# Optimization experiments

Measured on AMD Instinct MI355X. Metric: run time of the kernel, lower is better.

Reference implementation:

```python
import jax, jax.numpy as jnp
import numpy as np

NEG_BIG = -9e15


def setup_inputs() -> dict:
    key = jax.random.key(0)
    k1, k2, k3, k4 = jax.random.split(key, 4)
    B, N, F_in, F_out = 8, 2048, 512, 256
    x = jax.random.normal(k1, (B, N, F_in), dtype=jnp.float32)
    adj = jax.random.randint(k2, (B, N, N), 0, 2, dtype=jnp.int32)
    W = jax.random.normal(k3, (F_in, F_out), dtype=jnp.float32) * (1.414 / np.sqrt(F_in))
    a = jax.random.normal(k4, (2 * F_out, 1), dtype=jnp.float32) * 0.1
    return {"x": x, "adj": adj, "W": W, "a": a}


def reference(x, adj, W, a):
    # x: [B,N,Fin], adj: [B,N,N] int mask, W: [Fin,Fout], a: [2*Fout,1]
    alpha = 0.2  # LeakyReLU negative slope
    F_out = W.shape[1]
    h = jnp.einsum('bnf,fo->bno', x, W)              # [B,N,Fout]
    a1 = a[:F_out, 0]                                # [Fout]
    a2 = a[F_out:, 0]                                # [Fout]
    # e_ij = LeakyReLU([h_i || h_j] . a) = LeakyReLU(h_i.a1 + h_j.a2)
    f = h @ a1                                       # [B,N]
    g = h @ a2                                       # [B,N]
    e = jax.nn.leaky_relu(f[:, :, None] + g[:, None, :], negative_slope=alpha)  # [B,N,N]
    e = jnp.where(adj > 0, e, NEG_BIG)
    attention = jax.nn.softmax(e, axis=2)            # row-wise over neighbors j
    h_prime = jnp.einsum('bij,bjo->bio', attention, h)  # [B,N,Fout]
    return jax.nn.elu(h_prime)                       # concat=True path
```

## Files before the change

### kernel.cpp

```cpp
#include <hip/hip_runtime.h>
#include <math.h>

#define BATCH 8
#define NN    2048
#define FIN   512
#define FOUT  256
#define NEG_BIG -9000000000000000.0f

typedef __attribute__((ext_vector_type(8))) short bf16x8;
typedef __attribute__((ext_vector_type(4))) float f32x4;

__device__ __forceinline__ unsigned short f2bf(float x) {
    unsigned u = __float_as_uint(x);
    u = (u + 0x7FFF + ((u >> 16) & 1)) >> 16;
    return (unsigned short)u;
}
__device__ __forceinline__ float bf2f(unsigned short h) {
    return __uint_as_float(((unsigned)h) << 16);
}

__global__ __launch_bounds__(256) void wt_prep(const float* __restrict__ W,
                                               unsigned short* __restrict__ Wt_hi,
                                               unsigned short* __restrict__ Wt_lo) {
    const int tg = blockIdx.x * 256 + threadIdx.x;
    const int n  = tg >> 7;
    const int k4 = (tg & 127) * 4;
    unsigned short h[4], lo[4];
    #pragma unroll
    for (int i = 0; i < 4; i++) {
        const float v = W[(size_t)(k4 + i) * FOUT + n];
        h[i]  = f2bf(v);
        lo[i] = f2bf(v - bf2f(h[i]));
    }
    uint2 ph, pl;
    ph.x = h[0]  | ((unsigned)h[1]  << 16); ph.y = h[2]  | ((unsigned)h[3]  << 16);
    pl.x = lo[0] | ((unsigned)lo[1] << 16); pl.y = lo[2] | ((unsigned)lo[3] << 16);
    *(uint2*)(Wt_hi + (size_t)n * FIN + k4) = ph;
    *(uint2*)(Wt_lo + (size_t)n * FIN + k4) = pl;
}

__global__ __launch_bounds__(256, 2) void gemm_xw(const float* __restrict__ x,
        const unsigned short* __restrict__ Wt_hi,
        const unsigned short* __restrict__ Wt_lo,
        unsigned short* __restrict__ ht_hi,
        unsigned short* __restrict__ ht_lo) {
    __shared__ unsigned short As_hi[128][40];
    __shared__ unsigned short As_lo[128][40];
    const int t  = threadIdx.x;
    const int m0 = (blockIdx.x >> 2) * 128;
    const int n0 = (blockIdx.x & 3) * 64;
    const int l  = t & 63, w = t >> 6;
    const int wr = w >> 1, wc = w & 1;
    const int lr = l & 15, lk = l >> 4;

    f32x4 acc[4][2];
    #pragma unroll
    for (int mt = 0; mt < 4; mt++)
        #pragma unroll
        for (int nt = 0; nt < 2; nt++) acc[mt][nt] = (f32x4){0.f,0.f,0.f,0.f};

    for (int k0 = 0; k0 < FIN; k0 += 32) {
        float4 xv[4];
        #pragma unroll
        for (int r = 0; r < 4; r++) {
            const int fidx = t + 256*r, m = fidx >> 3, kq = fidx & 7;
            xv[r] = *(const float4*)(x + (size_t)(m0 + m) * FIN + k0 + kq*4);
        }
        bf16x8 bh[2], bl[2];
        #pragma unroll
        for (int nt = 0; nt < 2; nt++) {
            const size_t off = (size_t)(n0 + wc*32 + nt*16 + lr) * FIN + k0 + lk*8;
            bh[nt] = *(const bf16x8*)(Wt_hi + off);
            bl[nt] = *(const bf16x8*)(Wt_lo + off);
        }
        __syncthreads();
        #pragma unroll
        for (int r = 0; r < 4; r++) {
            const int fidx = t + 256*r, m = fidx >> 3, kq = fidx & 7;
            const float vv[4] = {xv[r].x, xv[r].y, xv[r].z, xv[r].w};
            unsigned short h[4], lo[4];
            #pragma unroll
            for (int i = 0; i < 4; i++) { h[i] = f2bf(vv[i]); lo[i] = f2bf(vv[i] - bf2f(h[i])); }
            uint2 ph, pl;
            ph.x = h[0]  | ((unsigned)h[1]  << 16); ph.y = h[2]  | ((unsigned)h[3]  << 16);
            pl.x = lo[0] | ((unsigned)lo[1] << 16); pl.y = lo[2] | ((unsigned)lo[3] << 16);
            *(uint2*)&As_hi[m][kq*4] = ph;
            *(uint2*)&As_lo[m][kq*4] = pl;
        }
        __syncthreads();
        bf16x8 ah[4], al[4];
        #pragma unroll
        for (int mt = 0; mt < 4; mt++) {
            const int row = wr*64 + mt*16 + lr;
            ah[mt] = *(const bf16x8*)&As_hi[row][lk*8];
            al[mt] = *(const bf16x8*)&As_lo[row][lk*8];
        }
        #pragma unroll
        for (int nt = 0; nt < 2; nt++)
            #pragma unroll
            for (int mt = 0; mt < 4; mt++)
                acc[mt][nt] = __builtin_amdgcn_mfma_f32_16x16x32_bf16(ah[mt], bh[nt], acc[mt][nt], 0, 0, 0);
        #pragma unroll
        for (int nt = 0; nt < 2; nt++)
            #pragma unroll
            for (int mt = 0; mt < 4; mt++)
                acc[mt][nt] = __builtin_amdgcn_mfma_f32_16x16x32_bf16(ah[mt], bl[nt], acc[mt][nt], 0, 0, 0);
        #pragma unroll
        for (int nt = 0; nt < 2; nt++)
            #pragma unroll
            for (int mt = 0; mt < 4; mt++)
                acc[mt][nt] = __builtin_amdgcn_mfma_f32_16x16x32_bf16(al[mt], bh[nt], acc[mt][nt], 0, 0, 0);
    }

    #pragma unroll
    for (int mt = 0; mt < 4; mt++)
        #pragma unroll
        for (int nt = 0; nt < 2; nt++) {
            const int n  = n0 + wc*32 + nt*16 + lr;
            const int mb = m0 + wr*64 + mt*16 + lk*4;
            const int bb = mb >> 11, jj = mb & 2047;
            const float av[4] = {acc[mt][nt].x, acc[mt][nt].y, acc[mt][nt].z, acc[mt][nt].w};
            unsigned short h[4], lo[4];
            #pragma unroll
            for (int r = 0; r < 4; r++) { h[r] = f2bf(av[r]); lo[r] = f2bf(av[r] - bf2f(h[r])); }
            uint2 ph, pl;
            ph.x = h[0]  | ((unsigned)h[1]  << 16); ph.y = h[2]  | ((unsigned)h[3]  << 16);
            pl.x = lo[0] | ((unsigned)lo[1] << 16); pl.y = lo[2] | ((unsigned)lo[3] << 16);
            const size_t base = ((size_t)bb * FOUT + n) * NN + jj;
            *(uint2*)(ht_hi + base) = ph;
            *(uint2*)(ht_lo + base) = pl;
        }
}

__global__ __launch_bounds__(256) void fg2(const unsigned short* __restrict__ ht_hi,
                                           const unsigned short* __restrict__ ht_lo,
                                           const float* __restrict__ a,
                                           float* __restrict__ f, float* __restrict__ g) {
    const int lane  = threadIdx.x & 63;
    const int chunk = blockIdx.x * 4 + (threadIdx.x >> 6);
    const int b  = chunk >> 5;
    const int jw = (chunk & 31) * 64 + lane;
    const size_t base = (size_t)b * FOUT * NN + jw;
    float fs = 0.f, gs = 0.f;
    #pragma unroll 4
    for (int n = 0; n < FOUT; n++) {
        const float hv = bf2f(ht_hi[base + (size_t)n * NN]) + bf2f(ht_lo[base + (size_t)n * NN]);
        fs = fmaf(hv, a[n], fs);
        gs = fmaf(hv, a[FOUT + n], gs);
    }
    f[b * NN + jw] = fs;
    g[b * NN + jw] = gs;
}

__global__ __launch_bounds__(256, 1) void gat_attn(
        const unsigned short* __restrict__ ht_hi,
        const unsigned short* __restrict__ ht_lo,
        const int* __restrict__ adj,
        const float* __restrict__ f, const float* __restrict__ g,
        float* __restrict__ out) {
    __shared__ unsigned short Hs_hi[256][72];
    __shared__ unsigned short Hs_lo[256][72];
    __shared__ unsigned short Ps_hi[64][72];
    __shared__ unsigned short Ps_lo[64][72];
    __shared__ __attribute__((aligned(16))) float m_s[64];
    __shared__ __attribute__((aligned(16))) float l_s[64];
    __shared__ __attribute__((aligned(16))) float fac_s[64];

    const int b  = blockIdx.x & 7;
    const int i0 = (blockIdx.x >> 3) * 64;
    const int t  = threadIdx.x;
    const int w  = t >> 6, l = t & 63;
    const int lr = l & 15, lk = l >> 4;
    const int ar = t >> 2, jg = t & 3;
    const float fi = f[b * NN + i0 + ar];

    if (t < 64) { m_s[t] = -INFINITY; l_s[t] = 0.f; }

    f32x4 acc[4][4];
    #pragma unroll
    for (int mt = 0; mt < 4; mt++)
        #pragma unroll
        for (int nt = 0; nt < 4; nt++) acc[mt][nt] = (f32x4){0.f,0.f,0.f,0.f};

    const unsigned short* hb_hi = ht_hi + (size_t)b * FOUT * NN;
    const unsigned short* hb_lo = ht_lo + (size_t)b * FOUT * NN;

    for (int jt = 0; jt < 32; jt++) {
        const int j0 = jt * 64;
        __syncthreads();

        {
            const int sn = t >> 3, sp = t & 7;
            #pragma unroll
            for (int p8 = 0; p8 < 8; p8++) {
                const int n = sn + p8 * 32;
                const size_t goff = (size_t)n * NN + j0 + sp * 8;
                const uint4 vh = *(const uint4*)(hb_hi + goff);
                const uint4 vl = *(const uint4*)(hb_lo + goff);
                *(uint4*)&Hs_hi[n][sp * 8] = vh;
                *(uint4*)&Hs_lo[n][sp * 8] = vl;
            }
        }

        {
            float s[16];
            float mloc = -INFINITY;
            const size_t arow = ((size_t)b * NN + i0 + ar) * NN + j0 + jg * 16;
            #pragma unroll
            for (int c = 0; c < 4; c++) {
                const int4   av = *(const int4*)(adj + arow + c * 4);
                const float4 gv = *(const float4*)(g + b * NN + j0 + jg * 16 + c * 4);
                const float v0 = fi + gv.x, v1 = fi + gv.y, v2 = fi + gv.z, v3 = fi + gv.w;
                s[c*4+0] = av.x > 0 ? (v0 > 0.f ? v0 : 0.2f * v0) : NEG_BIG;
                s[c*4+1] = av.y > 0 ? (v1 > 0.f ? v1 : 0.2f * v1) : NEG_BIG;
                s[c*4+2] = av.z > 0 ? (v2 > 0.f ? v2 : 0.2f * v2) : NEG_BIG;
                s[c*4+3] = av.w > 0 ? (v3 > 0.f ? v3 : 0.2f * v3) : NEG_BIG;
            }
            #pragma unroll
            for (int e = 0; e < 16; e++) mloc = fmaxf(mloc, s[e]);
            mloc = fmaxf(mloc, __shfl_xor(mloc, 1));
            mloc = fmaxf(mloc, __shfl_xor(mloc, 2));
            const float m_old = m_s[ar];
            const float m_new = fmaxf(m_old, mloc);
            float p[16], rs = 0.f;
            #pragma unroll
            for (int e = 0; e < 16; e++) { p[e] = __expf(s[e] - m_new); rs += p[e]; }
            rs += __shfl_xor(rs, 1);
            rs += __shfl_xor(rs, 2);
            if (jg == 0) {
                const float fac = __expf(m_old - m_new);
                fac_s[ar] = fac;
                l_s[ar]   = l_s[ar] * fac + rs;
                m_s[ar]   = m_new;
            }
            unsigned ph[8], pl[8];
            #pragma unroll
            for (int e = 0; e < 16; e += 2) {
                const unsigned short h0 = f2bf(p[e]),   h1 = f2bf(p[e+1]);
                const unsigned short q0 = f2bf(p[e] - bf2f(h0));
                const unsigned short q1 = f2bf(p[e+1] - bf2f(h1));
                ph[e >> 1] = h0 | ((unsigned)h1 << 16);
                pl[e >> 1] = q0 | ((unsigned)q1 << 16);
            }
            *(uint4*)&Ps_hi[ar][jg*16]     = make_uint4(ph[0], ph[1], ph[2], ph[3]);
            *(uint4*)&Ps_hi[ar][jg*16 + 8] = make_uint4(ph[4], ph[5], ph[6], ph[7]);
            *(uint4*)&Ps_lo[ar][jg*16]     = make_uint4(pl[0], pl[1], pl[2], pl[3]);
            *(uint4*)&Ps_lo[ar][jg*16 + 8] = make_uint4(pl[4], pl[5], pl[6], pl[7]);
        }
        __syncthreads();

        #pragma unroll
        for (int mt = 0; mt < 4; mt++) {
            const f32x4 fac4 = *(const f32x4*)&fac_s[mt*16 + lk*4];
            #pragma unroll
            for (int nt = 0; nt < 4; nt++) acc[mt][nt] *= fac4;
        }
        #pragma unroll
        for (int kt = 0; kt < 2; kt++) {
            bf16x8 ah[4], al[4], bh[4], bl[4];
            #pragma unroll
            for (int mt = 0; mt < 4; mt++) {
                ah[mt] = *(const bf16x8*)&Ps_hi[mt*16 + lr][kt*32 + lk*8];
                al[mt] = *(const bf16x8*)&Ps_lo[mt*16 + lr][kt*32 + lk*8];
            }
            #pragma unroll
            for (int nt = 0; nt < 4; nt++) {
                const int n = w*64 + nt*16 + lr;
                bh[nt] = *(const bf16x8*)&Hs_hi[n][kt*32 + lk*8];
                bl[nt] = *(const bf16x8*)&Hs_lo[n][kt*32 + lk*8];
            }
            #pragma unroll
            for (int nt = 0; nt < 4; nt++)
                #pragma unroll
                for (int mt = 0; mt < 4; mt++)
                    acc[mt][nt] = __builtin_amdgcn_mfma_f32_16x16x32_bf16(ah[mt], bh[nt], acc[mt][nt], 0, 0, 0);
            #pragma unroll
            for (int nt = 0; nt < 4; nt++)
                #pragma unroll
                for (int mt = 0; mt < 4; mt++)
                    acc[mt][nt] = __builtin_amdgcn_mfma_f32_16x16x32_bf16(ah[mt], bl[nt], acc[mt][nt], 0, 0, 0);
            #pragma unroll
            for (int nt = 0; nt < 4; nt++)
                #pragma unroll
                for (int mt = 0; mt < 4; mt++)
                    acc[mt][nt] = __builtin_amdgcn_mfma_f32_16x16x32_bf16(al[mt], bh[nt], acc[mt][nt], 0, 0, 0);
        }
    }

    __syncthreads();
    #pragma unroll
    for (int mt = 0; mt < 4; mt++) {
        const f32x4 lv = *(const f32x4*)&l_s[mt*16 + lk*4];
        const float linv[4] = {1.f/lv.x, 1.f/lv.y, 1.f/lv.z, 1.f/lv.w};
        const float av0[4][4] = {
            {acc[mt][0].x, acc[mt][0].y, acc[mt][0].z, acc[mt][0].w},
            {acc[mt][1].x, acc[mt][1].y, acc[mt][1].z, acc[mt][1].w},
            {acc[mt][2].x, acc[mt][2].y, acc[mt][2].z, acc[mt][2].w},
            {acc[mt][3].x, acc[mt][3].y, acc[mt][3].z, acc[mt][3].w}};
        #pragma unroll
        for (int nt = 0; nt < 4; nt++) {
            const int n = w*64 + nt*16 + lr;
            #pragma unroll
            for (int r = 0; r < 4; r++) {
                float v = av0[nt][r] * linv[r];
                v = v > 0.f ? v : (__expf(v) - 1.f);
                out[((size_t)(b * NN + i0 + mt*16 + lk*4 + r)) * FOUT + n] = v;
            }
        }
    }
}

extern "C" void kernel_launch(void* const* d_in, const int* in_sizes, int n_in,
                              void* d_out, int out_size, void* d_ws, size_t ws_size,
                              hipStream_t stream) {
    const float* x   = (const float*)d_in[0];
    const int*   adj = (const int*)  d_in[1];
    const float* W   = (const float*)d_in[2];
    const float* a   = (const float*)d_in[3];
    float* outp = (float*)d_out;

    char* ws = (char*)d_ws;
    unsigned short* ht_hi = (unsigned short*)ws;                       ws += (size_t)BATCH*FOUT*NN*2;
    unsigned short* ht_lo = (unsigned short*)ws;                       ws += (size_t)BATCH*FOUT*NN*2;
    unsigned short* Wt_hi = (unsigned short*)ws;                       ws += (size_t)FOUT*FIN*2;
    unsigned short* Wt_lo = (unsigned short*)ws;                       ws += (size_t)FOUT*FIN*2;
    float* f = (float*)ws;                                             ws += (size_t)BATCH*NN*4;
    float* g = (float*)ws;

    wt_prep <<<128, 256, 0, stream>>>(W, Wt_hi, Wt_lo);
    gemm_xw <<<512, 256, 0, stream>>>(x, Wt_hi, Wt_lo, ht_hi, ht_lo);
    fg2     <<<64,  256, 0, stream>>>(ht_hi, ht_lo, a, f, g);
    gat_attn<<<256, 256, 0, stream>>>(ht_hi, ht_lo, adj, f, g, outp);
}
```

Measured before the change: 354.5 us.

## Use 512-thread attention blocks with direct-to-LDS loads, swizzled LDS and prefetched adjacency

The attention kernel now runs 8 waves per block in a 2x4 wave grid. It stages the H tile with global_load_lds straight into XOR-swizzled unpadded LDS, and register-prefetches the next adjacency and g tile while the MFMAs run. The GEMM epilogue now transposes through LDS so the ht stores are 16-byte coalesced rows instead of scattered 8-byte writes. The aim is higher occupancy, fewer bank conflicts and overlap of the adjacency stream with compute, at the cost of more registers and extra barriers.

New measurement: 320.5 us. -9.6%, faster.

```diff
diff --git a/kernel.cpp b/kernel.cpp
--- a/kernel.cpp
+++ b/kernel.cpp
@@ -17,6 +17,11 @@
 }
 __device__ __forceinline__ float bf2f(unsigned short h) {
     return __uint_as_float(((unsigned)h) << 16);
+}
+__device__ __forceinline__ void gload_lds16(const void* g, void* l) {
+    __builtin_amdgcn_global_load_lds((const __attribute__((address_space(1))) void*)g,
+                                     (__attribute__((address_space(3))) void*)l,
+                                     16, 0, 0);
 }
 
 __global__ __launch_bounds__(256) void wt_prep(const float* __restrict__ W,
@@ -46,6 +51,7 @@
         unsigned short* __restrict__ ht_lo) {
     __shared__ unsigned short As_hi[128][40];
     __shared__ unsigned short As_lo[128][40];
+    __shared__ __attribute__((aligned(16))) unsigned short Tr[64][136];
     const int t  = threadIdx.x;
     const int m0 = (blockIdx.x >> 2) * 128;
     const int n0 = (blockIdx.x & 3) * 64;
@@ -112,24 +118,35 @@
                 acc[mt][nt] = __builtin_amdgcn_mfma_f32_16x16x32_bf16(al[mt], bh[nt], acc[mt][nt], 0, 0, 0);
     }
 
-    #pragma unroll
-    for (int mt = 0; mt < 4; mt++)
-        #pragma unroll
-        for (int nt = 0; nt < 2; nt++) {
-            const int n  = n0 + wc*32 + nt*16 + lr;
-            const int mb = m0 + wr*64 + mt*16 + lk*4;
-            const int bb = mb >> 11, jj = mb & 2047;
-            const float av[4] = {acc[mt][nt].x, acc[mt][nt].y, acc[mt][nt].z, acc[mt][nt].w};
-            unsigned short h[4], lo[4];
-            #pragma unroll
-            for (int r = 0; r < 4; r++) { h[r] = f2bf(av[r]); lo[r] = f2bf(av[r] - bf2f(h[r])); }
-            uint2 ph, pl;
-            ph.x = h[0]  | ((unsigned)h[1]  << 16); ph.y = h[2]  | ((unsigned)h[3]  << 16);
-            pl.x = lo[0] | ((unsigned)lo[1] << 16); pl.y = lo[2] | ((unsigned)lo[3] << 16);
-            const size_t base = ((size_t)bb * FOUT + n) * NN + jj;
-            *(uint2*)(ht_hi + base) = ph;
-            *(uint2*)(ht_lo + base) = pl;
-        }
+    const int bb  = m0 >> 11;
+    const int jj0 = m0 & 2047;
+    for (int pass = 0; pass < 2; pass++) {
+        #pragma unroll
+        for (int mt = 0; mt < 4; mt++)
+            #pragma unroll
+            for (int nt = 0; nt < 2; nt++) {
+                const int nl = wc*32 + nt*16 + lr;
+                const int ml = wr*64 + mt*16 + lk*4;
+                const float vv[4] = {acc[mt][nt].x, acc[mt][nt].y, acc[mt][nt].z, acc[mt][nt].w};
+                unsigned short s[4];
+                #pragma unroll
+                for (int r = 0; r < 4; r++) {
+                    const unsigned short hh = f2bf(vv[r]);
+                    s[r] = pass ? f2bf(vv[r] - bf2f(hh)) : hh;
+                }
+                *(unsigned*)&Tr[nl][ml]     = s[0] | ((unsigned)s[1] << 16);
+                *(unsigned*)&Tr[nl][ml + 2] = s[2] | ((unsigned)s[3] << 16);
+            }
+        __syncthreads();
+        unsigned short* dst = pass ? ht_lo : ht_hi;
+        #pragma unroll
+        for (int q = 0; q < 4; q++) {
+            const int idx = t + 256*q, row = idx >> 4, c = idx & 15;
+            *(uint4*)(dst + ((size_t)(bb * FOUT + n0 + row)) * NN + jj0 + c*8) =
+                *(const uint4*)&Tr[row][c*8];
+        }
+        __syncthreads();
+    }
 }
 
 __global__ __launch_bounds__(256) void fg2(const unsigned short* __restrict__ ht_hi,
@@ -152,16 +169,16 @@
     g[b * NN + jw] = gs;
 }
 
-__global__ __launch_bounds__(256, 1) void gat_attn(
+__global__ __launch_bounds__(512, 1) void gat_attn(
         const unsigned short* __restrict__ ht_hi,
         const unsigned short* __restrict__ ht_lo,
         const int* __restrict__ adj,
         const float* __restrict__ f, const float* __restrict__ g,
         float* __restrict__ out) {
-    __shared__ unsigned short Hs_hi[256][72];
-    __shared__ unsigned short Hs_lo[256][72];
-    __shared__ unsigned short Ps_hi[64][72];
-    __shared__ unsigned short Ps_lo[64][72];
+    __shared__ __attribute__((aligned(16))) unsigned short Hs_hi[256*64];
+    __shared__ __attribute__((aligned(16))) unsigned short Hs_lo[256*64];
+    __shared__ __attribute__((aligned(16))) unsigned short Ps_hi[64*64];
+    __shared__ __attribute__((aligned(16))) unsigned short Ps_lo[64*64];
     __shared__ __attribute__((aligned(16))) float m_s[64];
     __shared__ __attribute__((aligned(16))) float l_s[64];
     __shared__ __attribute__((aligned(16))) float fac_s[64];
@@ -171,140 +188,156 @@
     const int t  = threadIdx.x;
     const int w  = t >> 6, l = t & 63;
     const int lr = l & 15, lk = l >> 4;
-    const int ar = t >> 2, jg = t & 3;
+    const int wr = w >> 2, wc = w & 3;
+    const int ar = t >> 3, jg = t & 7;
+
     const float fi = f[b * NN + i0 + ar];
-
     if (t < 64) { m_s[t] = -INFINITY; l_s[t] = 0.f; }
 
-    f32x4 acc[4][4];
+    f32x4 acc[2][4];
     #pragma unroll
-    for (int mt = 0; mt < 4; mt++)
+    for (int mt = 0; mt < 2; mt++)
         #pragma unroll
         for (int nt = 0; nt < 4; nt++) acc[mt][nt] = (f32x4){0.f,0.f,0.f,0.f};
 
     const unsigned short* hb_hi = ht_hi + (size_t)b * FOUT * NN;
     const unsigned short* hb_lo = ht_lo + (size_t)b * FOUT * NN;
+    const size_t arow = ((size_t)b * NN + i0 + ar) * NN + jg * 8;
+    const float* grow = g + b * NN + jg * 8;
+
+    int4   adjA = *(const int4*)(adj + arow);
+    int4   adjB = *(const int4*)(adj + arow + 4);
+    float4 gA   = *(const float4*)(grow);
+    float4 gB   = *(const float4*)(grow + 4);
+
+    const int sidx = w * 4;
 
     for (int jt = 0; jt < 32; jt++) {
+        __syncthreads();
+
         const int j0 = jt * 64;
-        __syncthreads();
+        #pragma unroll
+        for (int q = 0; q < 4; q++) {
+            const int idx = (sidx + q) * 64 + l;
+            const int n = idx >> 3, c = idx & 7;
+            const int cc = c ^ (n & 7);
+            const size_t go = (size_t)n * NN + j0 + cc * 8;
+            gload_lds16(hb_hi + go, &Hs_hi[(sidx + q) * 512]);
+            gload_lds16(hb_lo + go, &Hs_lo[(sidx + q) * 512]);
+        }
 
         {
-            const int sn = t >> 3, sp = t & 7;
-            #pragma unroll
-            for (int p8 = 0; p8 < 8; p8++) {
-                const int n = sn + p8 * 32;
-                const size_t goff = (size_t)n * NN + j0 + sp * 8;
-                const uint4 vh = *(const uint4*)(hb_hi + goff);
-                const uint4 vl = *(const uint4*)(hb_lo + goff);
-                *(uint4*)&Hs_hi[n][sp * 8] = vh;
-                *(uint4*)&Hs_lo[n][sp * 8] = vl;
-            }
-        }
-
-        {
-            float s[16];
-            float mloc = -INFINITY;
-            const size_t arow = ((size_t)b * NN + i0 + ar) * NN + j0 + jg * 16;
-            #pragma unroll
-            for (int c = 0; c < 4; c++) {
-                const int4   av = *(const int4*)(adj + arow + c * 4);
-                const float4 gv = *(const float4*)(g + b * NN + j0 + jg * 16 + c * 4);
-                const float v0 = fi + gv.x, v1 = fi + gv.y, v2 = fi + gv.z, v3 = fi + gv.w;
-                s[c*4+0] = av.x > 0 ? (v0 > 0.f ? v0 : 0.2f * v0) : NEG_BIG;
-                s[c*4+1] = av.y > 0 ? (v1 > 0.f ? v1 : 0.2f * v1) : NEG_BIG;
-                s[c*4+2] = av.z > 0 ? (v2 > 0.f ? v2 : 0.2f * v2) : NEG_BIG;
-                s[c*4+3] = av.w > 0 ? (v3 > 0.f ? v3 : 0.2f * v3) : NEG_BIG;
-            }
-            #pragma unroll
-            for (int e = 0; e < 16; e++) mloc = fmaxf(mloc, s[e]);
+            float s[8];
+            {
+                const float v0 = fi + gA.x, v1 = fi + gA.y, v2 = fi + gA.z, v3 = fi + gA.w;
+                const float v4 = fi + gB.x, v5 = fi + gB.y, v6 = fi + gB.z, v7 = fi + gB.w;
+                s[0] = adjA.x > 0 ? (v0 > 0.f ? v0 : 0.2f*v0) : NEG_BIG;
+                s[1] = adjA.y > 0 ? (v1 > 0.f ? v1 : 0.2f*v1) : NEG_BIG;
+                s[2] = adjA.z > 0 ? (v2 > 0.f ? v2 : 0.2f*v2) : NEG_BIG;
+                s[3] = adjA.w > 0 ? (v3 > 0.f ? v3 : 0.2f*v3) : NEG_BIG;
+                s[4] = adjB.x > 0 ? (v4 > 0.f ? v4 : 0.2f*v4) : NEG_BIG;
+                s[5] = adjB.y > 0 ? (v5 > 0.f ? v5 : 0.2f*v5) : NEG_BIG;
+                s[6] = adjB.z > 0 ? (v6 > 0.f ? v6 : 0.2f*v6) : NEG_BIG;
+                s[7] = adjB.w > 0 ? (v7 > 0.f ? v7 : 0.2f*v7) : NEG_BIG;
+            }
+            float mloc = s[0];
+            #pragma unroll
+            for (int e = 1; e < 8; e++) mloc = fmaxf(mloc, s[e]);
             mloc = fmaxf(mloc, __shfl_xor(mloc, 1));
             mloc = fmaxf(mloc, __shfl_xor(mloc, 2));
+            mloc = fmaxf(mloc, __shfl_xor(mloc, 4));
             const float m_old = m_s[ar];
             const float m_new = fmaxf(m_old, mloc);
-            float p[16], rs = 0.f;
-            #pragma unroll
-            for (int e = 0; e < 16; e++) { p[e] = __expf(s[e] - m_new); rs += p[e]; }
+            float p[8], rs = 0.f;
+            #pragma unroll
+            for (int e = 0; e < 8; e++) { p[e] = __expf(s[e] - m_new); rs += p[e]; }
             rs += __shfl_xor(rs, 1);
             rs += __shfl_xor(rs, 2);
+            rs += __shfl_xor(rs, 4);
             if (jg == 0) {
                 const float fac = __expf(m_old - m_new);
                 fac_s[ar] = fac;
                 l_s[ar]   = l_s[ar] * fac + rs;
                 m_s[ar]   = m_new;
             }
-            unsigned ph[8], pl[8];
-            #pragma unroll
-            for (int e = 0; e < 16; e += 2) {
+            unsigned ph[4], pl[4];
+            #pragma unroll
+            for (int e = 0; e < 8; e += 2) {
                 const unsigned short h0 = f2bf(p[e]),   h1 = f2bf(p[e+1]);
                 const unsigned short q0 = f2bf(p[e] - bf2f(h0));
                 const unsigned short q1 = f2bf(p[e+1] - bf2f(h1));
                 ph[e >> 1] = h0 | ((unsigned)h1 << 16);
                 pl[e >> 1] = q0 | ((unsigned)q1 << 16);
             }
-            *(uint4*)&Ps_hi[ar][jg*16]     = make_uint4(ph[0], ph[1], ph[2], ph[3]);
-            *(uint4*)&Ps_hi[ar][jg*16 + 8] = make_uint4(ph[4], ph[5], ph[6], ph[7]);
-            *(uint4*)&Ps_lo[ar][jg*16]     = make_uint4(pl[0], pl[1], pl[2], pl[3]);
-            *(uint4*)&Ps_lo[ar][jg*16 + 8] = make_uint4(pl[4], pl[5], pl[6], pl[7]);
-        }
-        __syncthreads();
-
-        #pragma unroll
-        for (int mt = 0; mt < 4; mt++) {
-            const f32x4 fac4 = *(const f32x4*)&fac_s[mt*16 + lk*4];
+            const int cs = (jg ^ (ar & 7)) * 8;
+            *(uint4*)&Ps_hi[ar * 64 + cs] = make_uint4(ph[0], ph[1], ph[2], ph[3]);
+            *(uint4*)&Ps_lo[ar * 64 + cs] = make_uint4(pl[0], pl[1], pl[2], pl[3]);
+        }
+        __syncthreads();
+
+        if (jt + 1 < 32) {
+            const size_t o = (size_t)(jt + 1) * 64;
+            adjA = *(const int4*)(adj + arow + o);
+            adjB = *(const int4*)(adj + arow + o + 4);
+            gA   = *(const float4*)(grow + o);
+            gB   = *(const float4*)(grow + o + 4);
+        }
+
+        #pragma unroll
+        for (int mt = 0; mt < 2; mt++) {
+            const f32x4 fac4 = *(const f32x4*)&fac_s[wr*32 + mt*16 + lk*4];
             #pragma unroll
             for (int nt = 0; nt < 4; nt++) acc[mt][nt] *= fac4;
         }
         #pragma unroll
         for (int kt = 0; kt < 2; kt++) {
-            bf16x8 ah[4], al[4], bh[4], bl[4];
-            #pragma unroll
-            for (int mt = 0; mt < 4; mt++) {
-                ah[mt] = *(const bf16x8*)&Ps_hi[mt*16 + lr][kt*32 + lk*8];
-                al[mt] = *(const bf16x8*)&Ps_lo[mt*16 + lr][kt*32 + lk*8];
+            bf16x8 ah[2], al[2], bh[4], bl[4];
+            #pragma unroll
+            for (int mt = 0; mt < 2; mt++) {
+                const int row = wr*32 + mt*16 + lr;
+                const int cs  = ((kt*4 + lk) ^ (row & 7)) * 8;
+                ah[mt] = *(const bf16x8*)&Ps_hi[row * 64 + cs];
+                al[mt] = *(const bf16x8*)&Ps_lo[row * 64 + cs];
             }
             #pragma unroll
             for (int nt = 0; nt < 4; nt++) {
-                const int n = w*64 + nt*16 + lr;
-                bh[nt] = *(const bf16x8*)&Hs_hi[n][kt*32 + lk*8];
-                bl[nt] = *(const bf16x8*)&Hs_lo[n][kt*32 + lk*8];
+                const int n  = wc*64 + nt*16 + lr;
+                const int cs = ((kt*4 + lk) ^ (n & 7)) * 8;
+                bh[nt] = *(const bf16x8*)&Hs_hi[n * 64 + cs];
+                bl[nt] = *(const bf16x8*)&Hs_lo[n * 64 + cs];
             }
             #pragma unroll
             for (int nt = 0; nt < 4; nt++)
                 #pragma unroll
-                for (int mt = 0; mt < 4; mt++)
+                for (int mt = 0; mt < 2; mt++)
                     acc[mt][nt] = __builtin_amdgcn_mfma_f32_16x16x32_bf16(ah[mt], bh[nt], acc[mt][nt], 0, 0, 0);
             #pragma unroll
             for (int nt = 0; nt < 4; nt++)
                 #pragma unroll
-                for (int mt = 0; mt < 4; mt++)
+                for (int mt = 0; mt < 2; mt++)
                     acc[mt][nt] = __builtin_amdgcn_mfma_f32_16x16x32_bf16(ah[mt], bl[nt], acc[mt][nt], 0, 0, 0);
             #pragma unroll
             for (int nt = 0; nt < 4; nt++)
                 #pragma unroll
-                for (int mt = 0; mt < 4; mt++)
+                for (int mt = 0; mt < 2; mt++)
                     acc[mt][nt] = __builtin_amdgcn_mfma_f32_16x16x32_bf16(al[mt], bh[nt], acc[mt][nt], 0, 0, 0);
         }
     }
 
     __syncthreads();
     #pragma unroll
-    for (int mt = 0; mt < 4; mt++) {
-        const f32x4 lv = *(const f32x4*)&l_s[mt*16 + lk*4];
+    for (int mt = 0; mt < 2; mt++) {
+        const f32x4 lv = *(const f32x4*)&l_s[wr*32 + mt*16 + lk*4];
         const float linv[4] = {1.f/lv.x, 1.f/lv.y, 1.f/lv.z, 1.f/lv.w};
-        const float av0[4][4] = {
-            {acc[mt][0].x, acc[mt][0].y, acc[mt][0].z, acc[mt][0].w},
-            {acc[mt][1].x, acc[mt][1].y, acc[mt][1].z, acc[mt][1].w},
-            {acc[mt][2].x, acc[mt][2].y, acc[mt][2].z, acc[mt][2].w},
-            {acc[mt][3].x, acc[mt][3].y, acc[mt][3].z, acc[mt][3].w}};
         #pragma unroll
         for (int nt = 0; nt < 4; nt++) {
-            const int n = w*64 + nt*16 + lr;
+            const int n = wc*64 + nt*16 + lr;
+            const float av[4] = {acc[mt][nt].x, acc[mt][nt].y, acc[mt][nt].z, acc[mt][nt].w};
             #pragma unroll
             for (int r = 0; r < 4; r++) {
-                float v = av0[nt][r] * linv[r];
+                float v = av[r] * linv[r];
                 v = v > 0.f ? v : (__expf(v) - 1.f);
-                out[((size_t)(b * NN + i0 + mt*16 + lk*4 + r)) * FOUT + n] = v;
+                out[((size_t)(b * NN + i0 + wr*32 + mt*16 + lk*4 + r)) * FOUT + n] = v;
             }
         }
     }
@@ -330,5 +363,5 @@
     wt_prep <<<128, 256, 0, stream>>>(W, Wt_hi, Wt_lo);
     gemm_xw <<<512, 256, 0, stream>>>(x, Wt_hi, Wt_lo, ht_hi, ht_lo);
     fg2     <<<64,  256, 0, stream>>>(ht_hi, ht_lo, a, f, g);
-    gat_attn<<<256, 256, 0, stream>>>(ht_hi, ht_lo, adj, f, g, outp);
-}
+    gat_attn<<<256, 512, 0, stream>>>(ht_hi, ht_lo, adj, f, g, outp);
+}
```
